# Kernel tuning notes

Hardware: AMD Instinct MI355X
Metric: run time of the kernel (lower is better)

Reference implementation:

```python
import jax, jax.numpy as jnp
import numpy as np

N_NODES = 100000
N_EDGES = 1250000
D = 64


def _mlp(h, W1, b1, W2, b2):
    # shared GIN 'network': Linear -> ReLU -> Linear
    return jnp.maximum(h @ W1 + b1, 0.0) @ W2 + b2


def setup_inputs() -> dict:
    key = jax.random.key(0)
    ks = jax.random.split(key, 8)
    s = 1.0 / np.sqrt(D)
    x = jax.random.normal(ks[0], (N_NODES, D), dtype=jnp.float32)
    edge_index = jax.random.randint(ks[1], (2, N_EDGES), 0, N_NODES, dtype=jnp.int32)
    edge_attr = jax.random.normal(ks[2], (N_EDGES, D), dtype=jnp.float32)
    W1 = jax.random.normal(ks[3], (D, D), dtype=jnp.float32) * s
    b1 = jnp.zeros((D,), dtype=jnp.float32)
    W2 = jax.random.normal(ks[4], (D, D), dtype=jnp.float32) * s
    b2 = jnp.zeros((D,), dtype=jnp.float32)
    W_lin = jax.random.normal(ks[5], (3 * D, D), dtype=jnp.float32) * (1.0 / np.sqrt(3 * D))
    b_lin = jnp.zeros((D,), dtype=jnp.float32)
    return {"x": x, "edge_index": edge_index, "edge_attr": edge_attr,
            "W1": W1, "b1": b1, "W2": W2, "b2": b2,
            "W_lin": W_lin, "b_lin": b_lin}


def reference(x, edge_index, edge_attr, W1, b1, W2, b2, W_lin, b_lin):
    src = edge_index[0]  # [E]
    dst = edge_index[1]  # [E]
    n = x.shape[0]
    # forward conv: message from src -> aggregate at dst
    msg_f = jnp.maximum(x[src] + edge_attr, 0.0)            # [E, D]
    a_in = _mlp(jax.ops.segment_sum(msg_f, dst, num_segments=n), W1, b1, W2, b2)
    # backward conv (edge_index.flipud): message from dst -> aggregate at src
    msg_b = jnp.maximum(x[dst] + edge_attr, 0.0)            # [E, D]
    a_out = _mlp(jax.ops.segment_sum(msg_b, src, num_segments=n), W1, b1, W2, b2)
    # final projection of concat [x, a_in, a_out]
    return jnp.concatenate([x, a_in, a_out], axis=1) @ W_lin + b_lin
```

## Files before the change

### kernel.cpp

```cpp
#include <hip/hip_runtime.h>

#define NN 100000
#define NE 1250000
#define DD 64
#define NBKT 391
#define NCNT NBKT
#define NCNT2 (2 * NCNT)
#define CHUNK 8192
#define NCHUNK ((NE + CHUNK - 1) / CHUNK)
#define SORT_CAP 4096
#define GNB 25000
#define TSTR 68

typedef __attribute__((ext_vector_type(8))) short bf16x8_t;
typedef __attribute__((ext_vector_type(4))) float f32x4_t;

__device__ __forceinline__ unsigned short bf16_rne(float v) {
  unsigned u = __builtin_bit_cast(unsigned, v);
  u += 0x7FFFu + ((u >> 16) & 1u);
  return (unsigned short)(u >> 16);
}
__device__ __forceinline__ void split_bf16(float v, unsigned short& hi,
                                           unsigned short& lo) {
  hi = bf16_rne(v);
  const float fh = __builtin_bit_cast(float, ((unsigned)hi) << 16);
  lo = bf16_rne(v - fh);
}

__global__ __launch_bounds__(256) void precompute_kernel(
    const float* __restrict__ W2, const float* __restrict__ b2,
    const float* __restrict__ Wl, const float* __restrict__ bl,
    float* __restrict__ Wc1, float* __restrict__ Wc2, float* __restrict__ bc) {
  const int t = blockIdx.x * 256 + threadIdx.x;
  const int m = t >> 12;
  const int ij = t & 4095;
  const int i = ij >> 6, j = ij & 63;
  const float* Wp = Wl + (m ? 128 : 64) * 64;
  float s = 0.f;
#pragma unroll 8
  for (int k = 0; k < 64; ++k) s = fmaf(W2[i * 64 + k], Wp[k * 64 + j], s);
  if (m) Wc2[ij] = s; else Wc1[ij] = s;
  if (t < 64) {
    float sb = bl[t];
    for (int k = 0; k < 64; ++k)
      sb = fmaf(b2[k], Wl[(64 + k) * 64 + t] + Wl[(128 + k) * 64 + t], sb);
    bc[t] = sb;
  }
}

__global__ __launch_bounds__(256) void pack_w_kernel(
    const float* __restrict__ W1, const float* __restrict__ Wl,
    const float* __restrict__ Wc1, const float* __restrict__ Wc2,
    unsigned short* __restrict__ whi, unsigned short* __restrict__ wlo) {
  const int g = blockIdx.x * 256 + threadIdx.x;
  if (g >= 4 * 4096) return;
  const int mat = g >> 12;
  const int idx = g & 4095;
  const int i = idx & 7;
  const int lane = (idx >> 3) & 63;
  const int ct = (idx >> 9) & 3;
  const int ks = (idx >> 11) & 1;
  const int k = ks * 32 + ((lane >> 4) << 2) + (i & 3) + ((i >> 2) << 4);
  const int col = ct * 16 + (lane & 15);
  const float* src = (mat == 0) ? W1 : (mat == 1) ? Wc1 : (mat == 2) ? Wc2 : Wl;
  const float v = src[k * 64 + col];
  unsigned short h, l;
  split_bf16(v, h, l);
  whi[g] = h;
  wlo[g] = l;
}

__global__ __launch_bounds__(256) void multisplit_kernel(
    const int* __restrict__ ei, int* __restrict__ bcur2,
    int* __restrict__ tmp) {
  __shared__ int recs[CHUNK];
  __shared__ int hist[NBKT];
  __shared__ int hbase[NBKT + 1];
  __shared__ int hcur[NBKT];
  __shared__ int gbase[NBKT];
  __shared__ int scanbuf[256];
  const int t = threadIdx.x;
  const int dir = (blockIdx.x >= NCHUNK) ? 1 : 0;
  const int chunk = blockIdx.x - (dir ? NCHUNK : 0);
  const int e0 = chunk * CHUNK;
  const int cnt = min(CHUNK, NE - e0);
  const int* keys = ei + (dir ? 0 : NE);
  for (int i = t; i < NBKT; i += 256) {
    hist[i] = 0;
    hcur[i] = 0;
  }
  __syncthreads();
  for (int i = t; i < cnt; i += 256) atomicAdd(&hist[keys[e0 + i] >> 8], 1);
  __syncthreads();
  const int i0 = 2 * t, i1 = 2 * t + 1;
  const int s0 = (i0 < NBKT) ? hist[i0] : 0;
  const int s1 = (i1 < NBKT) ? hist[i1] : 0;
  const int ps = s0 + s1;
  scanbuf[t] = ps;
  __syncthreads();
  int acc = ps;
  for (int d = 1; d < 256; d <<= 1) {
    const int add = (t >= d) ? scanbuf[t - d] : 0;
    __syncthreads();
    acc += add;
    scanbuf[t] = acc;
    __syncthreads();
  }
  const int pre = acc - ps;
  if (i0 < NBKT) hbase[i0] = pre;
  if (i1 < NBKT) hbase[i1] = pre + s0;
  if (t == 0) hbase[NBKT] = cnt;
  __syncthreads();
  for (int b = t; b < NBKT; b += 256) {
    const int c = hist[b];
    if (c > 0)
      gbase[b] = (dir * NBKT + b) * SORT_CAP +
                 atomicAdd(&bcur2[dir * NBKT + b], c);
  }
  for (int i = t; i < cnt; i += 256) {
    const int n = keys[e0 + i];
    const int b = n >> 8;
    const int p = hbase[b] + atomicAdd(&hcur[b], 1);
    recs[p] = ((e0 + i) << 8) | (n & 255);
  }
  __syncthreads();
  for (int p = t; p < cnt; p += 256) {
    int lo = 0, hi = NBKT;
    while (hi - lo > 1) {
      const int mid = (lo + hi) >> 1;
      if (hbase[mid] <= p) lo = mid;
      else hi = mid;
    }
    tmp[gbase[lo] + (p - hbase[lo])] = recs[p];
  }
}

__global__ __launch_bounds__(256) void bucket_sort_kernel(
    const int* __restrict__ tmp, const int* __restrict__ bcur2,
    const int* __restrict__ ei, int* __restrict__ offb_d,
    int* __restrict__ offe_d, int* __restrict__ offb_s,
    int* __restrict__ offe_s, int2* __restrict__ lst2) {
  __shared__ int hist[256];
  __shared__ int scanbuf[256];
  __shared__ int cur[256];
  const int t = threadIdx.x;
  const int isrc = (blockIdx.x >= NBKT) ? 1 : 0;
  const int bloc = blockIdx.x - (isrc ? NBKT : 0);
  const int base = (isrc * NBKT + bloc) * SORT_CAP;
  const int cnt = min(bcur2[isrc * NCNT + bloc], SORT_CAP);
  const int* pbase = ei + (isrc ? NE : 0);
  hist[t] = 0;
  __syncthreads();
  for (int k = t; k < cnt; k += 256) atomicAdd(&hist[tmp[base + k] & 255], 1);
  __syncthreads();
  const int v = hist[t];
  int acc = v;
  scanbuf[t] = v;
  __syncthreads();
  for (int d = 1; d < 256; d <<= 1) {
    const int add = (t >= d) ? scanbuf[t - d] : 0;
    __syncthreads();
    acc += add;
    scanbuf[t] = acc;
    __syncthreads();
  }
  const int beg_t = base + acc - v;
  cur[t] = beg_t;
  int* offb = isrc ? offb_s : offb_d;
  int* offe = isrc ? offe_s : offe_d;
  const int n = bloc * 256 + t;
  if (n < NN) {
    offb[n] = beg_t;
    offe[n] = base + acc;
  }
  __syncthreads();
  for (int k = t; k < cnt; k += 256) {
    const int r = tmp[base + k];
    const int e = (int)(((unsigned)r) >> 8);
    const int p = atomicAdd(&cur[r & 255], 1);
    lst2[p] = make_int2(e, pbase[e]);
  }
}

__global__ __launch_bounds__(256) void gather_kernel(
    const float* __restrict__ x, const float* __restrict__ ea,
    const int* __restrict__ offb_d, const int* __restrict__ offe_d,
    const int* __restrict__ offb_s, const int* __restrict__ offe_s,
    const int2* __restrict__ lst2, float* __restrict__ agg_in,
    float* __restrict__ agg_out) {
  const int t = threadIdx.x;
  const int wave = t >> 6;
  const int lane = t & 63;
  const int slot = lane >> 3;
  const int q = lane & 7;
  const int dir = (blockIdx.x >= GNB) ? 1 : 0;
  const int n = (blockIdx.x - (dir ? GNB : 0)) * 4 + wave;
  if (n >= NN) return;
  const int* offb = dir ? offb_s : offb_d;
  const int* offe = dir ? offe_s : offe_d;
  float* agg = dir ? agg_out : agg_in;
  const int beg = offb[n];
  const int end = offe[n];
  const int c0 = q * 8;
  float4 acc0 = make_float4(0.f, 0.f, 0.f, 0.f);
  float4 acc1 = make_float4(0.f, 0.f, 0.f, 0.f);
  for (int k = beg + slot; k < end; k += 8) {
    const int2 r = lst2[k];
    const float* ar = ea + (size_t)r.x * DD + c0;
    const float* xr = x + (size_t)r.y * DD + c0;
    const float4 a0 = *reinterpret_cast<const float4*>(ar);
    const float4 a1 = *reinterpret_cast<const float4*>(ar + 4);
    const float4 x0 = *reinterpret_cast<const float4*>(xr);
    const float4 x1 = *reinterpret_cast<const float4*>(xr + 4);
    acc0.x += fmaxf(a0.x + x0.x, 0.f);
    acc0.y += fmaxf(a0.y + x0.y, 0.f);
    acc0.z += fmaxf(a0.z + x0.z, 0.f);
    acc0.w += fmaxf(a0.w + x0.w, 0.f);
    acc1.x += fmaxf(a1.x + x1.x, 0.f);
    acc1.y += fmaxf(a1.y + x1.y, 0.f);
    acc1.z += fmaxf(a1.z + x1.z, 0.f);
    acc1.w += fmaxf(a1.w + x1.w, 0.f);
  }
#pragma unroll
  for (int m = 8; m <= 32; m <<= 1) {
    acc0.x += __shfl_xor(acc0.x, m);
    acc0.y += __shfl_xor(acc0.y, m);
    acc0.z += __shfl_xor(acc0.z, m);
    acc0.w += __shfl_xor(acc0.w, m);
    acc1.x += __shfl_xor(acc1.x, m);
    acc1.y += __shfl_xor(acc1.y, m);
    acc1.z += __shfl_xor(acc1.z, m);
    acc1.w += __shfl_xor(acc1.w, m);
  }
  if (lane < 8) {
    float* p = agg + (size_t)n * DD + lane * 8;
    *reinterpret_cast<float4*>(p) = acc0;
    *reinterpret_cast<float4*>(p + 4) = acc1;
  }
}

__global__ __launch_bounds__(256) void edge_kernel(
    const float* __restrict__ x, const int* __restrict__ ei,
    const float* __restrict__ ea, float* __restrict__ agg_in,
    float* __restrict__ agg_out) {
  const int tid = blockIdx.x * 256 + threadIdx.x;
  const int e = tid >> 4;
  if (e >= NE) return;
  const int c = (tid & 15) * 4;
  const int s = ei[e];
  const int d = ei[NE + e];
  const float4 a = *reinterpret_cast<const float4*>(ea + (size_t)e * DD + c);
  const float4 xs = *reinterpret_cast<const float4*>(x + (size_t)s * DD + c);
  const float4 xd = *reinterpret_cast<const float4*>(x + (size_t)d * DD + c);
  float* pi = agg_in + (size_t)d * DD + c;
  unsafeAtomicAdd(pi + 0, fmaxf(xs.x + a.x, 0.f));
  unsafeAtomicAdd(pi + 1, fmaxf(xs.y + a.y, 0.f));
  unsafeAtomicAdd(pi + 2, fmaxf(xs.z + a.z, 0.f));
  unsafeAtomicAdd(pi + 3, fmaxf(xs.w + a.w, 0.f));
  float* po = agg_out + (size_t)s * DD + c;
  unsafeAtomicAdd(po + 0, fmaxf(xd.x + a.x, 0.f));
  unsafeAtomicAdd(po + 1, fmaxf(xd.y + a.y, 0.f));
  unsafeAtomicAdd(po + 2, fmaxf(xd.z + a.z, 0.f));
  unsafeAtomicAdd(po + 3, fmaxf(xd.w + a.w, 0.f));
}

__device__ __forceinline__ void mm_pass(const float* At, int wv, int lane,
                                        const unsigned short* __restrict__ whi,
                                        const unsigned short* __restrict__ wlo,
                                        int mat, f32x4_t acc[4]) {
  const int row = (wv << 4) + (lane & 15);
  const int kbase = ((lane >> 4) & 3) << 2;
#pragma unroll
  for (int ks = 0; ks < 2; ++ks) {
    const float* ap = At + row * TSTR + ks * 32 + kbase;
    const float4 g0 = *reinterpret_cast<const float4*>(ap);
    const float4 g1 = *reinterpret_cast<const float4*>(ap + 16);
    const float gv[8] = {g0.x, g0.y, g0.z, g0.w, g1.x, g1.y, g1.z, g1.w};
    bf16x8_t ahi, alo;
#pragma unroll
    for (int i = 0; i < 8; ++i) {
      unsigned short h, l;
      split_bf16(gv[i], h, l);
      ahi[i] = (short)h;
      alo[i] = (short)l;
    }
#pragma unroll
    for (int ct = 0; ct < 4; ++ct) {
      const int fb = ((mat * 2 + ks) * 4 + ct) * 512 + lane * 8;
      const bf16x8_t wh = *reinterpret_cast<const bf16x8_t*>(whi + fb);
      const bf16x8_t wl = *reinterpret_cast<const bf16x8_t*>(wlo + fb);
      acc[ct] = __builtin_amdgcn_mfma_f32_16x16x32_bf16(ahi, wh, acc[ct], 0, 0, 0);
      acc[ct] = __builtin_amdgcn_mfma_f32_16x16x32_bf16(alo, wh, acc[ct], 0, 0, 0);
      acc[ct] = __builtin_amdgcn_mfma_f32_16x16x32_bf16(ahi, wl, acc[ct], 0, 0, 0);
    }
  }
}

__global__ __launch_bounds__(256) void node_kernel(
    const float* __restrict__ x, const float* __restrict__ agg_in,
    const float* __restrict__ agg_out, const float* __restrict__ b1,
    const float* __restrict__ bc, const unsigned short* __restrict__ whi,
    const unsigned short* __restrict__ wlo, float* __restrict__ out) {
  __shared__ float TA[64 * TSTR];
  __shared__ float TH[64 * TSTR];
  const int t = threadIdx.x;
  const int lane = t & 63;
  const int wv = t >> 6;
  const int n0 = blockIdx.x * 64;

  f32x4_t ofrag[4];
#pragma unroll
  for (int ct = 0; ct < 4; ++ct) ofrag[ct] = (f32x4_t){0.f, 0.f, 0.f, 0.f};
  float b1v[4], bcv[4];
#pragma unroll
  for (int ct = 0; ct < 4; ++ct) {
    b1v[ct] = b1[ct * 16 + (lane & 15)];
    bcv[ct] = bc[ct * 16 + (lane & 15)];
  }

#define LOAD_TILE_F32(SRC)                                                    \
  {                                                                           \
    const int r = t >> 2;                                                     \
    const int cb = (t & 3) * 16;                                              \
    const int n = n0 + r;                                                     \
    _Pragma("unroll") for (int ii = 0; ii < 4; ++ii) {                        \
      float4 v = make_float4(0.f, 0.f, 0.f, 0.f);                             \
      if (n < NN)                                                             \
        v = *reinterpret_cast<const float4*>((SRC) + (size_t)n * DD + cb +    \
                                             ii * 4);                         \
      *reinterpret_cast<float4*>(&TA[r * TSTR + cb + ii * 4]) = v;            \
    }                                                                         \
  }

#define H_PASS(MATW1)                                                         \
  {                                                                           \
    f32x4_t h[4];                                                             \
    _Pragma("unroll") for (int ct = 0; ct < 4; ++ct) h[ct] =                  \
        (f32x4_t){0.f, 0.f, 0.f, 0.f};                                        \
    mm_pass(TA, wv, lane, whi, wlo, (MATW1), h);                              \
    _Pragma("unroll") for (int ct = 0; ct < 4; ++ct)                          \
        _Pragma("unroll") for (int r = 0; r < 4; ++r) {                       \
      const float hv = fmaxf(h[ct][r] + b1v[ct], 0.f);                        \
      TH[((wv << 4) + ((lane >> 4) << 2) + r) * TSTR + ct * 16 +              \
         (lane & 15)] = hv;                                                   \
    }                                                                         \
  }

  LOAD_TILE_F32(agg_in);
  __syncthreads();
  H_PASS(0);
  __syncthreads();
  mm_pass(TH, wv, lane, whi, wlo, 1, ofrag);
  __syncthreads();
  LOAD_TILE_F32(agg_out);
  __syncthreads();
  H_PASS(0);
  __syncthreads();
  mm_pass(TH, wv, lane, whi, wlo, 2, ofrag);
  __syncthreads();
  LOAD_TILE_F32(x);
  __syncthreads();
  mm_pass(TA, wv, lane, whi, wlo, 3, ofrag);

#pragma unroll
  for (int ct = 0; ct < 4; ++ct)
#pragma unroll
    for (int r = 0; r < 4; ++r) {
      const int n = n0 + (wv << 4) + ((lane >> 4) << 2) + r;
      if (n < NN)
        out[(size_t)n * DD + ct * 16 + (lane & 15)] = ofrag[ct][r] + bcv[ct];
    }
}

extern "C" void kernel_launch(void* const* d_in, const int* in_sizes, int n_in,
                              void* d_out, int out_size, void* d_ws,
                              size_t ws_size, hipStream_t stream) {
  const float* x = (const float*)d_in[0];
  const int* ei = (const int*)d_in[1];
  const float* ea = (const float*)d_in[2];
  const float* W1 = (const float*)d_in[3];
  const float* b1 = (const float*)d_in[4];
  const float* W2 = (const float*)d_in[5];
  const float* b2 = (const float*)d_in[6];
  const float* Wl = (const float*)d_in[7];
  const float* bl = (const float*)d_in[8];
  float* out = (float*)d_out;
  float* ws = (float*)d_ws;

  const size_t REG = (size_t)NCNT2 * SORT_CAP;
  float* agg_in = ws;
  float* agg_out = agg_in + (size_t)NN * DD;
  int* tmp = (int*)(agg_out + (size_t)NN * DD);
  int2* lst2 = (int2*)(tmp + REG);
  int* offb_d = (int*)(lst2 + REG);
  int* offe_d = offb_d + NN + 4;
  int* offb_s = offe_d + NN + 4;
  int* offe_s = offb_s + NN + 4;
  int* bcur2 = offe_s + NN + 4;
  float* Wc1 = (float*)(bcur2 + NCNT2 + 10);
  float* Wc2 = Wc1 + 4096;
  float* bc = Wc2 + 4096;
  unsigned short* whi = (unsigned short*)(bc + 64);
  unsigned short* wlo = whi + 4 * 4096;
  const size_t need = (size_t)((char*)(wlo + 4 * 4096) - (char*)ws);

  const bool bkt_ok = ws_size >= need;
  if (!bkt_ok) {
    Wc1 = agg_out + (size_t)NN * DD;
    Wc2 = Wc1 + 4096;
    bc = Wc2 + 4096;
    whi = (unsigned short*)(bc + 64);
    wlo = whi + 4 * 4096;
  }

  precompute_kernel<<<32, 256, 0, stream>>>(W2, b2, Wl, bl, Wc1, Wc2, bc);
  pack_w_kernel<<<64, 256, 0, stream>>>(W1, Wl, Wc1, Wc2, whi, wlo);

  if (bkt_ok) {
    hipMemsetAsync(bcur2, 0, NCNT2 * sizeof(int), stream);
    multisplit_kernel<<<2 * NCHUNK, 256, 0, stream>>>(ei, bcur2, tmp);
    bucket_sort_kernel<<<2 * NBKT, 256, 0, stream>>>(
        tmp, bcur2, ei, offb_d, offe_d, offb_s, offe_s, lst2);
    gather_kernel<<<2 * GNB, 256, 0, stream>>>(x, ea, offb_d, offe_d, offb_s,
                                               offe_s, lst2, agg_in, agg_out);
  } else {
    hipMemsetAsync(agg_in, 0, 2 * (size_t)NN * DD * sizeof(float), stream);
    edge_kernel<<<((size_t)NE * 16 + 255) / 256, 256, 0, stream>>>(
        x, ei, ea, agg_in, agg_out);
  }

  node_kernel<<<(NN + 63) / 64, 256, 0, stream>>>(x, agg_in, agg_out, b1, bc,
                                                  whi, wlo, out);
}
```

Measured before the change: 329.4 us.

## Carry partner node through multisplit records and widen bucket sort blocks

Multisplit records become int2 values holding the edge id plus the partner node packed with the low key byte, so bucket_sort no longer does a random gather into edge_index. The binary search over bucket bases is replaced by a stored per-record bucket id in shared memory. CHUNK is halved to keep shared memory in budget and give more blocks, and bucket_sort runs with 512 threads. The cost is double the intermediate tmp traffic and a larger workspace footprint, since tmp is now int2.

```diff
diff --git a/kernel.cpp b/kernel.cpp
--- a/kernel.cpp
+++ b/kernel.cpp
@@ -6,7 +6,7 @@
 #define NBKT 391
 #define NCNT NBKT
 #define NCNT2 (2 * NCNT)
-#define CHUNK 8192
+#define CHUNK 4096
 #define NCHUNK ((NE + CHUNK - 1) / CHUNK)
 #define SORT_CAP 4096
 #define GNB 25000
@@ -72,10 +72,11 @@
 
 __global__ __launch_bounds__(256) void multisplit_kernel(
     const int* __restrict__ ei, int* __restrict__ bcur2,
-    int* __restrict__ tmp) {
-  __shared__ int recs[CHUNK];
+    int2* __restrict__ tmp) {
+  __shared__ int2 recs[CHUNK];
+  __shared__ unsigned short rbkt[CHUNK];
   __shared__ int hist[NBKT];
-  __shared__ int hbase[NBKT + 1];
+  __shared__ int hbase[NBKT];
   __shared__ int hcur[NBKT];
   __shared__ int gbase[NBKT];
   __shared__ int scanbuf[256];
@@ -85,6 +86,7 @@
   const int e0 = chunk * CHUNK;
   const int cnt = min(CHUNK, NE - e0);
   const int* keys = ei + (dir ? 0 : NE);
+  const int* prt = ei + (dir ? NE : 0);
   for (int i = t; i < NBKT; i += 256) {
     hist[i] = 0;
     hcur[i] = 0;
@@ -109,7 +111,6 @@
   const int pre = acc - ps;
   if (i0 < NBKT) hbase[i0] = pre;
   if (i1 < NBKT) hbase[i1] = pre + s0;
-  if (t == 0) hbase[NBKT] = cnt;
   __syncthreads();
   for (int b = t; b < NBKT; b += 256) {
     const int c = hist[b];
@@ -121,25 +122,21 @@
     const int n = keys[e0 + i];
     const int b = n >> 8;
     const int p = hbase[b] + atomicAdd(&hcur[b], 1);
-    recs[p] = ((e0 + i) << 8) | (n & 255);
+    recs[p] = make_int2(e0 + i, (prt[e0 + i] << 8) | (n & 255));
+    rbkt[p] = (unsigned short)b;
   }
   __syncthreads();
   for (int p = t; p < cnt; p += 256) {
-    int lo = 0, hi = NBKT;
-    while (hi - lo > 1) {
-      const int mid = (lo + hi) >> 1;
-      if (hbase[mid] <= p) lo = mid;
-      else hi = mid;
-    }
-    tmp[gbase[lo] + (p - hbase[lo])] = recs[p];
-  }
-}
-
-__global__ __launch_bounds__(256) void bucket_sort_kernel(
-    const int* __restrict__ tmp, const int* __restrict__ bcur2,
-    const int* __restrict__ ei, int* __restrict__ offb_d,
-    int* __restrict__ offe_d, int* __restrict__ offb_s,
-    int* __restrict__ offe_s, int2* __restrict__ lst2) {
+    const int b = rbkt[p];
+    tmp[gbase[b] + (p - hbase[b])] = recs[p];
+  }
+}
+
+__global__ __launch_bounds__(512) void bucket_sort_kernel(
+    const int2* __restrict__ tmp, const int* __restrict__ bcur2,
+    int* __restrict__ offb_d, int* __restrict__ offe_d,
+    int* __restrict__ offb_s, int* __restrict__ offe_s,
+    int2* __restrict__ lst2) {
   __shared__ int hist[256];
   __shared__ int scanbuf[256];
   __shared__ int cur[256];
@@ -148,37 +145,43 @@
   const int bloc = blockIdx.x - (isrc ? NBKT : 0);
   const int base = (isrc * NBKT + bloc) * SORT_CAP;
   const int cnt = min(bcur2[isrc * NCNT + bloc], SORT_CAP);
-  const int* pbase = ei + (isrc ? NE : 0);
-  hist[t] = 0;
-  __syncthreads();
-  for (int k = t; k < cnt; k += 256) atomicAdd(&hist[tmp[base + k] & 255], 1);
-  __syncthreads();
-  const int v = hist[t];
-  int acc = v;
-  scanbuf[t] = v;
+  if (t < 256) hist[t] = 0;
+  __syncthreads();
+  for (int k = t; k < cnt; k += 512)
+    atomicAdd(&hist[tmp[base + k].y & 255], 1);
+  __syncthreads();
+  int v = 0, acc = 0;
+  if (t < 256) {
+    v = hist[t];
+    acc = v;
+    scanbuf[t] = v;
+  }
   __syncthreads();
   for (int d = 1; d < 256; d <<= 1) {
-    const int add = (t >= d) ? scanbuf[t - d] : 0;
+    int add = 0;
+    if (t < 256 && t >= d) add = scanbuf[t - d];
     __syncthreads();
-    acc += add;
-    scanbuf[t] = acc;
+    if (t < 256) {
+      acc += add;
+      scanbuf[t] = acc;
+    }
     __syncthreads();
   }
-  const int beg_t = base + acc - v;
-  cur[t] = beg_t;
-  int* offb = isrc ? offb_s : offb_d;
-  int* offe = isrc ? offe_s : offe_d;
-  const int n = bloc * 256 + t;
-  if (n < NN) {
-    offb[n] = beg_t;
-    offe[n] = base + acc;
-  }
-  __syncthreads();
-  for (int k = t; k < cnt; k += 256) {
-    const int r = tmp[base + k];
-    const int e = (int)(((unsigned)r) >> 8);
-    const int p = atomicAdd(&cur[r & 255], 1);
-    lst2[p] = make_int2(e, pbase[e]);
+  if (t < 256) {
+    cur[t] = base + acc - v;
+    int* offb = isrc ? offb_s : offb_d;
+    int* offe = isrc ? offe_s : offe_d;
+    const int n = bloc * 256 + t;
+    if (n < NN) {
+      offb[n] = base + acc - v;
+      offe[n] = base + acc;
+    }
+  }
+  __syncthreads();
+  for (int k = t; k < cnt; k += 512) {
+    const int2 r = tmp[base + k];
+    const int p = atomicAdd(&cur[r.y & 255], 1);
+    lst2[p] = make_int2(r.x, (int)(((unsigned)r.y) >> 8));
   }
 }
 
@@ -390,8 +393,8 @@
   const size_t REG = (size_t)NCNT2 * SORT_CAP;
   float* agg_in = ws;
   float* agg_out = agg_in + (size_t)NN * DD;
-  int* tmp = (int*)(agg_out + (size_t)NN * DD);
-  int2* lst2 = (int2*)(tmp + REG);
+  int2* tmp = (int2*)(agg_out + (size_t)NN * DD);
+  int2* lst2 = tmp + REG;
   int* offb_d = (int*)(lst2 + REG);
   int* offe_d = offb_d + NN + 4;
   int* offb_s = offe_d + NN + 4;
@@ -419,8 +422,8 @@
   if (bkt_ok) {
     hipMemsetAsync(bcur2, 0, NCNT2 * sizeof(int), stream);
     multisplit_kernel<<<2 * NCHUNK, 256, 0, stream>>>(ei, bcur2, tmp);
-    bucket_sort_kernel<<<2 * NBKT, 256, 0, stream>>>(
-        tmp, bcur2, ei, offb_d, offe_d, offb_s, offe_s, lst2);
+    bucket_sort_kernel<<<2 * NBKT, 512, 0, stream>>>(
+        tmp, bcur2, offb_d, offe_d, offb_s, offe_s, lst2);
     gather_kernel<<<2 * GNB, 256, 0, stream>>>(x, ea, offb_d, offe_d, offb_s,
                                                offe_s, lst2, agg_in, agg_out);
   } else {
```

Measured after the change: 288.4 us. -12.4%, faster.
